# Kernel tuning notes

Measured on AMD Instinct MI355X. Metric: run time of the kernel, lower is better.

## Reference

```python
import jax, jax.numpy as jnp
import numpy as np

N = 100000      # nodes (single ntype)
F_IN = 128
F_OUT = 128
R = 3           # relations
E = 262144      # edges per relation
LRELU_SLOPE = 0.2


def setup_inputs() -> dict:
    key = jax.random.key(0)
    ks = jax.random.split(key, 6)
    x = jax.random.normal(ks[0], (N, F_IN), jnp.float32)
    src = jax.random.randint(ks[1], (R, E), 0, N)
    dst = jax.random.randint(ks[2], (R, E), 0, N)
    # attention: Linear(2*in_feat, 1) per relation
    att_w = jax.random.normal(ks[3], (R, 2 * F_IN, 1), jnp.float32) * 0.05
    att_b = jnp.zeros((R, 1), jnp.float32)
    # transform: Linear(in_feat, out_feat) per relation
    tw = jax.random.normal(ks[4], (R, F_IN, F_OUT), jnp.float32) * (1.0 / np.sqrt(F_IN))
    tb = jnp.zeros((R, F_OUT), jnp.float32)
    h_bias = jnp.zeros((F_OUT,), jnp.float32)
    return dict(x=x, att_w=att_w, att_b=att_b, tw=tw, tb=tb,
                h_bias=h_bias, src=src, dst=dst)


def reference(x, att_w, att_b, tw, tb, h_bias, src, dst):
    # Per-relation gather of endpoint features.  [R, E, F_IN]
    h_src = x[src]
    h_dst = x[dst]
    # attention Linear on cat([h_src, h_dst]) == split matmul (avoids concat)
    w_s, w_d = att_w[:, :F_IN, :], att_w[:, F_IN:, :]
    scores = (jnp.einsum('ref,rfo->reo', h_src, w_s)
              + jnp.einsum('ref,rfo->reo', h_dst, w_d)
              + att_b[:, None, :])                      # [R, E, 1]
    scores = jax.nn.leaky_relu(scores, negative_slope=LRELU_SLOPE)
    # Faithful to source: F.softmax(scores, dim=0) -> softmax over ALL edges
    # of a relation (NOT per-destination edge softmax).
    a = jax.nn.softmax(scores, axis=1)                  # [R, E, 1]
    # u_mul_e with node-level transform(h_src): message = (h_src @ tw + tb) * a
    msg = (jnp.einsum('ref,rfo->reo', h_src, tw) + tb[:, None, :]) * a  # [R,E,F_OUT]
    # scatter-sum to destinations per relation, then sum over relations
    agg = jax.vmap(lambda m, d: jax.ops.segment_sum(m, d, num_segments=N))(msg, dst)
    h = agg.sum(axis=0) + h_bias                        # [N, F_OUT]
    # activation=relu, dropout=0.0 (identity)
    return jax.nn.relu(h)
```

## Files before the change

kernel.cpp:

```cpp
#include <hip/hip_runtime.h>
#include <hip/hip_bf16.h>

#define N_NODES 100000
#define FDIM 128
#define RREL 3
#define NEDGE 262144
#define SLOPE 0.2f
#define NCHUNK 98
#define PROJ_BLOCKS 782
#define HIST_BLOCKS (RREL * NEDGE / 256)

typedef __attribute__((ext_vector_type(8))) short bf16x8;
typedef __attribute__((ext_vector_type(8))) unsigned short u16x8;
typedef __attribute__((ext_vector_type(4))) float f32x4;
typedef __attribute__((ext_vector_type(16))) float f32x16;
typedef __attribute__((ext_vector_type(4))) int i32x4;

__device__ inline unsigned short f2bf(float f) {
    __hip_bfloat16 h = __float2bfloat16(f);
    return *reinterpret_cast<unsigned short*>(&h);
}
__device__ inline float bf2f(unsigned short u) {
    unsigned int b = ((unsigned int)u) << 16;
    return __int_as_float(b);
}

#define WS_PS    0
#define WS_PD    300000
#define WS_SUMS  600000
#define WS_COUNT 600016
#define WS_ROWS  900016
#define WS_BSUM  1200016
#define WS_ESORT 1200528
#define WS_ASUM  2773392
#define WS_TWT   3073392
#define WS_TBS   3097968
#define WS_XBF   3098352
#define WS_AGGB  9498352
#define WS_RANK  28698352

__global__ __launch_bounds__(256, 4)
void proj_hist_kernel(const float* __restrict__ x,
                      const float* __restrict__ att_w,
                      float* __restrict__ ps, float* __restrict__ pd,
                      unsigned short* __restrict__ x_bf,
                      const int* __restrict__ dst, int* __restrict__ count,
                      int* __restrict__ rank) {
    if (blockIdx.x >= PROJ_BLOCKS) {
        const int b = blockIdx.x - PROJ_BLOCKS;
        const int gid = b * 256 + threadIdx.x;
        const int r = b >> 10;
        rank[gid] = atomicAdd(&count[r * N_NODES + dst[gid]], 1);
        return;
    }
    __shared__ unsigned short sX[128 * 136];
    __shared__ unsigned short sW[16 * 136];
    const int tid = threadIdx.x;
    const int row0 = blockIdx.x * 128;

#pragma unroll
    for (int i = 0; i < 8; ++i) {
        const int idx = tid + i * 256;
        const int c = idx >> 7, k = idx & 127;
        float v = 0.f;
        if (c < 3) v = att_w[c * 256 + k];
        else if (c < 6) v = att_w[(c - 3) * 256 + 128 + k];
        sW[c * 136 + k] = f2bf(v);
    }
    const int g = tid >> 5, lane = tid & 31;
#pragma unroll
    for (int it = 0; it < 16; ++it) {
        const int rrow = it * 8 + g;
        const int row = row0 + rrow;
        float4 xv = make_float4(0.f, 0.f, 0.f, 0.f);
        if (row < N_NODES) xv = *reinterpret_cast<const float4*>(x + (size_t)row * FDIM + lane * 4);
        ushort4 u;
        u.x = f2bf(xv.x); u.y = f2bf(xv.y); u.z = f2bf(xv.z); u.w = f2bf(xv.w);
        if (row < N_NODES)
            *reinterpret_cast<ushort4*>(x_bf + (size_t)row * FDIM + lane * 4) = u;
        *reinterpret_cast<ushort4*>(&sX[rrow * 136 + lane * 4]) = u;
    }
    __syncthreads();

    const int w = tid >> 6, l = tid & 63;
    const int lr = l & 15, lk = l >> 4;
    f32x4 acc[2];
    acc[0] = (f32x4){0.f, 0.f, 0.f, 0.f};
    acc[1] = (f32x4){0.f, 0.f, 0.f, 0.f};
#pragma unroll
    for (int ks = 0; ks < 4; ++ks) {
        const bf16x8 bfr = *reinterpret_cast<const bf16x8*>(&sW[lr * 136 + ks * 32 + lk * 8]);
#pragma unroll
        for (int rt = 0; rt < 2; ++rt) {
            const bf16x8 afr =
                *reinterpret_cast<const bf16x8*>(&sX[(w * 32 + rt * 16 + lr) * 136 + ks * 32 + lk * 8]);
            acc[rt] = __builtin_amdgcn_mfma_f32_16x16x32_bf16(afr, bfr, acc[rt], 0, 0, 0);
        }
    }
    if (lr < 6) {
        float* base = (lr < 3) ? (ps + lr * N_NODES) : (pd + (lr - 3) * N_NODES);
#pragma unroll
        for (int rt = 0; rt < 2; ++rt) {
            const int rowbase = row0 + w * 32 + rt * 16 + lk * 4;
#pragma unroll
            for (int j = 0; j < 4; ++j) {
                const int row = rowbase + j;
                if (row < N_NODES) base[row] = acc[rt][j];
            }
        }
    }
}

__global__ void scan1_kernel(const int* __restrict__ count, int* __restrict__ row_start,
                             int* __restrict__ bsum) {
    const int r = blockIdx.x / NCHUNK;
    const int b = blockIdx.x % NCHUNK;
    const int tid = threadIdx.x;
    const int base = b * 1024 + tid * 4;
    int v[4];
#pragma unroll
    for (int i = 0; i < 4; ++i)
        v[i] = (base + i < N_NODES) ? count[r * N_NODES + base + i] : 0;
    const int tsum = v[0] + v[1] + v[2] + v[3];
    __shared__ int sd[256];
    sd[tid] = tsum;
    __syncthreads();
    for (int off = 1; off < 256; off <<= 1) {
        const int tv = (tid >= off) ? sd[tid - off] : 0;
        __syncthreads();
        sd[tid] += tv;
        __syncthreads();
    }
    int run = sd[tid] - tsum;
#pragma unroll
    for (int i = 0; i < 4; ++i) {
        if (base + i < N_NODES) row_start[r * N_NODES + base + i] = run;
        run += v[i];
    }
    if (tid == 255) bsum[blockIdx.x] = sd[255];
}

__global__ void scan2_kernel(int* __restrict__ bsum) {
    const int r = blockIdx.x;
    const int tid = threadIdx.x;
    const int v = (tid < NCHUNK) ? bsum[r * NCHUNK + tid] : 0;
    __shared__ int sd[256];
    sd[tid] = v;
    __syncthreads();
    for (int off = 1; off < 256; off <<= 1) {
        const int tv = (tid >= off) ? sd[tid - off] : 0;
        __syncthreads();
        sd[tid] += tv;
        __syncthreads();
    }
    if (tid < NCHUNK) bsum[r * NCHUNK + tid] = sd[tid] - v;
}

__global__ void scan3_kernel(int* __restrict__ row_start, const int* __restrict__ bsum) {
    const int r = blockIdx.x / NCHUNK;
    const int b = blockIdx.x % NCHUNK;
    const int add = bsum[blockIdx.x];
    const int base = b * 1024 + threadIdx.x * 4;
#pragma unroll
    for (int i = 0; i < 4; ++i)
        if (base + i < N_NODES) row_start[r * N_NODES + base + i] += add;
}

__global__ void fill_kernel(const int* __restrict__ src, const int* __restrict__ dst,
                            const float* __restrict__ ps, const float* __restrict__ pd,
                            const float* __restrict__ att_b,
                            const int* __restrict__ row_start, const int* __restrict__ rank,
                            int2* __restrict__ edge_sorted, float* __restrict__ sums) {
    const int gid = blockIdx.x * 256 + threadIdx.x;
    const int r = blockIdx.x >> 10;
    const int s = src[gid];
    const int d = dst[gid];
    float sc = ps[r * N_NODES + s] + pd[r * N_NODES + d] + att_b[r];
    sc = sc > 0.f ? sc : SLOPE * sc;
    const float ev = __expf(sc);
    const int pos = row_start[r * N_NODES + d] + rank[gid];
    int2 pk;
    pk.x = s;
    pk.y = __float_as_int(ev);
    edge_sorted[(size_t)r * NEDGE + pos] = pk;
    float v = ev;
#pragma unroll
    for (int off = 32; off >= 1; off >>= 1) v += __shfl_xor(v, off);
    __shared__ float red[4];
    if ((threadIdx.x & 63) == 0) red[threadIdx.x >> 6] = v;
    __syncthreads();
    if (threadIdx.x == 0) {
        unsafeAtomicAdd(&sums[r], red[0] + red[1] + red[2] + red[3]);
    }
}

__global__ void cast_kernel(const float* __restrict__ tw, const float* __restrict__ tb,
                            const float* __restrict__ sums,
                            unsigned short* __restrict__ twT, float* __restrict__ tbs) {
    const int o = blockIdx.x * 256 + threadIdx.x;
    const int elem = o & 7;
    const int lane = (o >> 3) & 63;
    const int ct   = (o >> 9) & 3;
    const int kk   = (o >> 11) & 1;
    const int ks   = o >> 12;
    const int col = ct * 32 + (lane & 31);
    const int k   = ks * 32 + kk * 16 + ((lane >> 5) << 3) + elem;
    const float inv = 1.0f / sums[k >> 7];
    twT[o] = f2bf(tw[k * 128 + col] * inv);
    if (o < 384) tbs[o] = tb[o] * (1.0f / sums[o >> 7]);
}

__global__ void agg_kernel(const int* __restrict__ row_start,
                           const int2* __restrict__ edge_sorted,
                           const unsigned short* __restrict__ x_bf,
                           unsigned short* __restrict__ aggb, float* __restrict__ asum) {
    const int lane = threadIdx.x & 15;
    const int r = blockIdx.y;
    const int n = blockIdx.x * 16 + (threadIdx.x >> 4);
    const int beg = row_start[r * N_NODES + n];
    const int end = (n == N_NODES - 1) ? NEDGE : row_start[r * N_NODES + n + 1];
    const long long* es = (const long long*)(edge_sorted + (size_t)r * NEDGE);

    float acc[8] = {0.f, 0.f, 0.f, 0.f, 0.f, 0.f, 0.f, 0.f};
    float asacc = 0.f;

    for (int i = beg; i < end; i += 4) {
        const int rem = end - i;
        long long q0, q1, q2, q3;
        q0 = __builtin_nontemporal_load(es + i);
        if (rem > 1) q1 = __builtin_nontemporal_load(es + i + 1);
        if (rem > 2) q2 = __builtin_nontemporal_load(es + i + 2);
        if (rem > 3) q3 = __builtin_nontemporal_load(es + i + 3);
        u16x8 xv0, xv1, xv2, xv3;
        xv0 = *reinterpret_cast<const u16x8*>(x_bf + (size_t)(int)q0 * FDIM + lane * 8);
        if (rem > 1) xv1 = *reinterpret_cast<const u16x8*>(x_bf + (size_t)(int)q1 * FDIM + lane * 8);
        if (rem > 2) xv2 = *reinterpret_cast<const u16x8*>(x_bf + (size_t)(int)q2 * FDIM + lane * 8);
        if (rem > 3) xv3 = *reinterpret_cast<const u16x8*>(x_bf + (size_t)(int)q3 * FDIM + lane * 8);
        {
            const float a = __int_as_float((int)(q0 >> 32));
            asacc += a;
#pragma unroll
            for (int d = 0; d < 8; ++d) acc[d] += a * bf2f(xv0[d]);
        }
        if (rem > 1) {
            const float a = __int_as_float((int)(q1 >> 32));
            asacc += a;
#pragma unroll
            for (int d = 0; d < 8; ++d) acc[d] += a * bf2f(xv1[d]);
        }
        if (rem > 2) {
            const float a = __int_as_float((int)(q2 >> 32));
            asacc += a;
#pragma unroll
            for (int d = 0; d < 8; ++d) acc[d] += a * bf2f(xv2[d]);
        }
        if (rem > 3) {
            const float a = __int_as_float((int)(q3 >> 32));
            asacc += a;
#pragma unroll
            for (int d = 0; d < 8; ++d) acc[d] += a * bf2f(xv3[d]);
        }
    }

    u16x8 o;
#pragma unroll
    for (int d = 0; d < 8; ++d) o[d] = f2bf(acc[d]);
    i32x4* dst4 = reinterpret_cast<i32x4*>(aggb + (size_t)n * 384 + r * FDIM + lane * 8);
    __builtin_nontemporal_store(*reinterpret_cast<i32x4*>(&o), dst4);
    if (lane == 0) asum[r * N_NODES + n] = asacc;
}

__global__ __launch_bounds__(128, 4)
void gemm_kernel(const unsigned short* __restrict__ A, const unsigned short* __restrict__ Bf,
                 const float* __restrict__ asum, const float* __restrict__ tbs,
                 const float* __restrict__ h_bias, float* __restrict__ out) {
    __shared__ int4 sB[2][512];
    const int tid = threadIdx.x;
    const int w = tid >> 6, l = tid & 63;
    const int row = l & 31, hi = l >> 5;
    const int n0 = blockIdx.x * 64 + w * 32;
    const int arow = min(n0 + row, N_NODES - 1);
    const unsigned short* aptr = A + (size_t)arow * 384 + hi * 8;
    const int4* Bfv = reinterpret_cast<const int4*>(Bf);

#pragma unroll
    for (int i = 0; i < 4; ++i) sB[0][i * 128 + tid] = Bfv[i * 128 + tid];
    bf16x8 af0 = *reinterpret_cast<const bf16x8*>(aptr);
    bf16x8 af1 = *reinterpret_cast<const bf16x8*>(aptr + 16);
    __syncthreads();

    f32x16 acc[4];
#pragma unroll
    for (int ct = 0; ct < 4; ++ct)
#pragma unroll
        for (int j = 0; j < 16; ++j) acc[ct][j] = 0.f;

    for (int ks = 0; ks < 12; ++ks) {
        const int buf = ks & 1;
        int4 rb[4];
        bf16x8 afn0, afn1;
        if (ks < 11) {
            const int base = (ks + 1) * 512;
#pragma unroll
            for (int i = 0; i < 4; ++i) rb[i] = Bfv[base + i * 128 + tid];
            afn0 = *reinterpret_cast<const bf16x8*>(aptr + (ks + 1) * 32);
            afn1 = *reinterpret_cast<const bf16x8*>(aptr + (ks + 1) * 32 + 16);
        }
        const unsigned short* sb = reinterpret_cast<const unsigned short*>(&sB[buf][0]);
#pragma unroll
        for (int ct = 0; ct < 4; ++ct) {
            const bf16x8 b0 = *reinterpret_cast<const bf16x8*>(sb + ct * 512 + l * 8);
            acc[ct] = __builtin_amdgcn_mfma_f32_32x32x16_bf16(af0, b0, acc[ct], 0, 0, 0);
        }
#pragma unroll
        for (int ct = 0; ct < 4; ++ct) {
            const bf16x8 b1 = *reinterpret_cast<const bf16x8*>(sb + 2048 + ct * 512 + l * 8);
            acc[ct] = __builtin_amdgcn_mfma_f32_32x32x16_bf16(af1, b1, acc[ct], 0, 0, 0);
        }
        if (ks < 11) {
#pragma unroll
            for (int i = 0; i < 4; ++i) sB[buf ^ 1][i * 128 + tid] = rb[i];
            af0 = afn0;
            af1 = afn1;
        }
        __syncthreads();
    }

    const int col = row;
    const float hb = h_bias[col];
    const float t0 = tbs[col], t1 = tbs[FDIM + col], t2 = tbs[2 * FDIM + col];
#pragma unroll
    for (int g = 0; g < 4; ++g) {
        const int rbase = n0 + g * 8 + hi * 4;
        float as0[4], as1[4], as2[4];
#pragma unroll
        for (int j = 0; j < 4; ++j) {
            const bool ok = (rbase + j) < N_NODES;
            as0[j] = ok ? asum[0 * N_NODES + rbase + j] : 0.f;
            as1[j] = ok ? asum[1 * N_NODES + rbase + j] : 0.f;
            as2[j] = ok ? asum[2 * N_NODES + rbase + j] : 0.f;
        }
#pragma unroll
        for (int ct = 0; ct < 4; ++ct) {
#pragma unroll
            for (int j = 0; j < 4; ++j) {
                const int r_ = rbase + j;
                if (r_ < N_NODES) {
                    float v = acc[ct][g * 4 + j] + as0[j] * t0 + as1[j] * t1 + as2[j] * t2 + hb;
                    out[(size_t)r_ * FDIM + ct * 32 + col] = fmaxf(v, 0.f);
                }
            }
        }
    }
}

extern "C" void kernel_launch(void* const* d_in, const int* in_sizes, int n_in,
                              void* d_out, int out_size, void* d_ws, size_t ws_size,
                              hipStream_t stream) {
    const float* x      = (const float*)d_in[0];
    const float* att_w  = (const float*)d_in[1];
    const float* att_b  = (const float*)d_in[2];
    const float* tw     = (const float*)d_in[3];
    const float* tb     = (const float*)d_in[4];
    const float* h_bias = (const float*)d_in[5];
    const int*   src    = (const int*)d_in[6];
    const int*   dst    = (const int*)d_in[7];
    float* out = (float*)d_out;

    float* wsf = (float*)d_ws;
    float* ps         = wsf + WS_PS;
    float* pd         = wsf + WS_PD;
    float* sums       = wsf + WS_SUMS;
    int*   count      = (int*)(wsf + WS_COUNT);
    int*   row_start  = (int*)(wsf + WS_ROWS);
    int*   bsum       = (int*)(wsf + WS_BSUM);
    int2*  edge_sorted= (int2*)(wsf + WS_ESORT);
    float* asum       = wsf + WS_ASUM;
    unsigned short* twT  = (unsigned short*)(wsf + WS_TWT);
    float* tbs        = wsf + WS_TBS;
    unsigned short* x_bf = (unsigned short*)(wsf + WS_XBF);
    unsigned short* aggb = (unsigned short*)(wsf + WS_AGGB);
    int*   rank       = (int*)(wsf + WS_RANK);

    hipMemsetAsync(sums, 0, 16 * sizeof(float), stream);
    hipMemsetAsync(count, 0, (size_t)RREL * N_NODES * sizeof(int), stream);

    proj_hist_kernel<<<PROJ_BLOCKS + HIST_BLOCKS, 256, 0, stream>>>(x, att_w, ps, pd, x_bf,
                                                                    dst, count, rank);

    scan1_kernel<<<RREL * NCHUNK, 256, 0, stream>>>(count, row_start, bsum);
    scan2_kernel<<<RREL, 256, 0, stream>>>(bsum);
    scan3_kernel<<<RREL * NCHUNK, 256, 0, stream>>>(row_start, bsum);

    fill_kernel<<<RREL * NEDGE / 256, 256, 0, stream>>>(src, dst, ps, pd, att_b,
                                                        row_start, rank, edge_sorted, sums);

    cast_kernel<<<192, 256, 0, stream>>>(tw, tb, sums, twT, tbs);

    agg_kernel<<<dim3(N_NODES / 16, RREL), 256, 0, stream>>>(row_start, edge_sorted, x_bf,
                                                             aggb, asum);

    gemm_kernel<<<(N_NODES + 63) / 64, 128, 0, stream>>>(aggb, twT, asum, tbs, h_bias, out);
}
```

Before: 206.0 us.

## Load full weight matrix into LDS once per large block in GEMM

```diff
diff --git a/kernel.cpp b/kernel.cpp
--- a/kernel.cpp
+++ b/kernel.cpp
@@ -270,24 +270,23 @@
     if (lane == 0) asum[r * N_NODES + n] = asacc;
 }
 
-__global__ __launch_bounds__(128, 4)
+__global__ __launch_bounds__(1024, 4)
 void gemm_kernel(const unsigned short* __restrict__ A, const unsigned short* __restrict__ Bf,
                  const float* __restrict__ asum, const float* __restrict__ tbs,
                  const float* __restrict__ h_bias, float* __restrict__ out) {
-    __shared__ int4 sB[2][512];
+    __shared__ int4 sB[6144];
     const int tid = threadIdx.x;
+    const int4* Bfv = reinterpret_cast<const int4*>(Bf);
+#pragma unroll
+    for (int i = 0; i < 6; ++i) sB[i * 1024 + tid] = Bfv[i * 1024 + tid];
+    __syncthreads();
+
     const int w = tid >> 6, l = tid & 63;
     const int row = l & 31, hi = l >> 5;
-    const int n0 = blockIdx.x * 64 + w * 32;
+    const int n0 = blockIdx.x * 512 + w * 32;
     const int arow = min(n0 + row, N_NODES - 1);
     const unsigned short* aptr = A + (size_t)arow * 384 + hi * 8;
-    const int4* Bfv = reinterpret_cast<const int4*>(Bf);
-
-#pragma unroll
-    for (int i = 0; i < 4; ++i) sB[0][i * 128 + tid] = Bfv[i * 128 + tid];
-    bf16x8 af0 = *reinterpret_cast<const bf16x8*>(aptr);
-    bf16x8 af1 = *reinterpret_cast<const bf16x8*>(aptr + 16);
-    __syncthreads();
+    const unsigned short* sb = reinterpret_cast<const unsigned short*>(sB);
 
     f32x16 acc[4];
 #pragma unroll
@@ -295,35 +294,21 @@
 #pragma unroll
         for (int j = 0; j < 16; ++j) acc[ct][j] = 0.f;
 
+#pragma unroll
     for (int ks = 0; ks < 12; ++ks) {
-        const int buf = ks & 1;
-        int4 rb[4];
-        bf16x8 afn0, afn1;
-        if (ks < 11) {
-            const int base = (ks + 1) * 512;
-#pragma unroll
-            for (int i = 0; i < 4; ++i) rb[i] = Bfv[base + i * 128 + tid];
-            afn0 = *reinterpret_cast<const bf16x8*>(aptr + (ks + 1) * 32);
-            afn1 = *reinterpret_cast<const bf16x8*>(aptr + (ks + 1) * 32 + 16);
-        }
-        const unsigned short* sb = reinterpret_cast<const unsigned short*>(&sB[buf][0]);
+        const bf16x8 af0 = *reinterpret_cast<const bf16x8*>(aptr + ks * 32);
+        const bf16x8 af1 = *reinterpret_cast<const bf16x8*>(aptr + ks * 32 + 16);
+        const unsigned short* sbk = sb + ks * 4096;
 #pragma unroll
         for (int ct = 0; ct < 4; ++ct) {
-            const bf16x8 b0 = *reinterpret_cast<const bf16x8*>(sb + ct * 512 + l * 8);
+            const bf16x8 b0 = *reinterpret_cast<const bf16x8*>(sbk + ct * 512 + l * 8);
             acc[ct] = __builtin_amdgcn_mfma_f32_32x32x16_bf16(af0, b0, acc[ct], 0, 0, 0);
         }
 #pragma unroll
         for (int ct = 0; ct < 4; ++ct) {
-            const bf16x8 b1 = *reinterpret_cast<const bf16x8*>(sb + 2048 + ct * 512 + l * 8);
+            const bf16x8 b1 = *reinterpret_cast<const bf16x8*>(sbk + 2048 + ct * 512 + l * 8);
             acc[ct] = __builtin_amdgcn_mfma_f32_32x32x16_bf16(af1, b1, acc[ct], 0, 0, 0);
         }
-        if (ks < 11) {
-#pragma unroll
-            for (int i = 0; i < 4; ++i) sB[buf ^ 1][i * 128 + tid] = rb[i];
-            af0 = afn0;
-            af1 = afn1;
-        }
-        __syncthreads();
     }
 
     const int col = row;
@@ -400,5 +385,5 @@
     agg_kernel<<<dim3(N_NODES / 16, RREL), 256, 0, stream>>>(row_start, edge_sorted, x_bf,
                                                              aggb, asum);
 
-    gemm_kernel<<<(N_NODES + 63) / 64, 128, 0, stream>>>(aggb, twT, asum, tbs, h_bias, out);
-}
+    gemm_kernel<<<196, 1024, 0, stream>>>(aggb, twT, asum, tbs, h_bias, out);
+}
```

After: 192.7 us. 1.07x faster.
